# Optimization experiments

Hardware: AMD Instinct MI355X
Metric: run time of the kernel (lower is better)

## Reference

```python
import jax, jax.numpy as jnp
import numpy as np

N = 100000      # nodes
E = 1600000     # edges (avg degree 16)
IN = 512        # input feature dim
H, C = 8, 8     # conv1: 8 heads x 8 channels (hardcoded in module)
HID = H * C     # 64
OUT = 64        # output classes (conv2: 1 head, no concat)
NEG_SLOPE = 0.2 # PyG GATConv default leaky-relu slope


def setup_inputs() -> dict:
    key = jax.random.key(0)
    ks = jax.random.split(key, 10)
    x = jax.random.normal(ks[0], (N, IN), dtype=jnp.float32)
    edge_index = jax.random.randint(ks[1], (2, E), 0, N, dtype=jnp.int32)
    W1 = jax.random.normal(ks[2], (IN, HID), dtype=jnp.float32) / np.sqrt(IN).astype(np.float32)
    a_src1 = jax.random.normal(ks[3], (H, C), dtype=jnp.float32) * 0.1
    a_dst1 = jax.random.normal(ks[4], (H, C), dtype=jnp.float32) * 0.1
    b1 = jnp.zeros((HID,), dtype=jnp.float32)
    W2 = jax.random.normal(ks[5], (HID, OUT), dtype=jnp.float32) / np.sqrt(HID).astype(np.float32)
    a_src2 = jax.random.normal(ks[6], (1, OUT), dtype=jnp.float32) * 0.1
    a_dst2 = jax.random.normal(ks[7], (1, OUT), dtype=jnp.float32) * 0.1
    b2 = jnp.zeros((OUT,), dtype=jnp.float32)
    return {"x": x, "edge_index": edge_index, "W1": W1, "a_src1": a_src1,
            "a_dst1": a_dst1, "b1": b1, "W2": W2, "a_src2": a_src2,
            "a_dst2": a_dst2, "b2": b2}


def _gat_attend(h, src, dst, a_s, a_d, n_nodes):
    """h: [N,H,C]; src/dst: [E]; a_s/a_d: [H,C] -> aggregated [N,H,C]."""
    # per-node half-scores (PyG decomposition of a^T [Wx_i || Wx_j])
    sc_s = jnp.sum(h * a_s, axis=-1)                       # [N,H]
    sc_d = jnp.sum(h * a_d, axis=-1)                       # [N,H]
    logits = jax.nn.leaky_relu(sc_s[src] + sc_d[dst], NEG_SLOPE)  # [E,H]
    # segment softmax over edges grouped by destination node
    mx = jax.ops.segment_max(logits, dst, num_segments=n_nodes)   # [N,H]
    ex = jnp.exp(logits - mx[dst])                          # [E,H]
    denom = jax.ops.segment_sum(ex, dst, num_segments=n_nodes)    # [N,H]
    alpha = ex / (denom[dst] + 1e-16)                       # [E,H]
    msg = h[src] * alpha[:, :, None]                        # [E,H,C]
    return jax.ops.segment_sum(msg, dst, num_segments=n_nodes)    # [N,H,C]


def reference(x, edge_index, W1, a_src1, a_dst1, b1, W2, a_src2, a_dst2, b2):
    n = x.shape[0]
    loop = jnp.arange(n, dtype=edge_index.dtype)
    src = jnp.concatenate([edge_index[0], loop])            # self-loops (PyG default)
    dst = jnp.concatenate([edge_index[1], loop])
    # conv1: 8 heads, concat
    h1 = (x @ W1).reshape(n, H, C)
    o1 = _gat_attend(h1, src, dst, a_src1, a_dst1, n).reshape(n, HID) + b1
    x2 = jax.nn.elu(o1)
    # conv2: 1 head, no concat
    h2 = (x2 @ W2).reshape(n, 1, OUT)
    o2 = _gat_attend(h2, src, dst, a_src2, a_dst2, n)[:, 0] + b2
    return jax.nn.log_softmax(o2, axis=1)
```

## Files before the change

### kernel.cpp

```cpp
#include <hip/hip_runtime.h>
#include <cstdint>
#include <cstddef>

#define LEAKY 0.2f
#define NEG_INF -3.402823466e38f
static const int CHUNK = 2048;

typedef __attribute__((ext_vector_type(8))) short short8;
typedef __attribute__((ext_vector_type(4))) float floatx4;

__device__ __forceinline__ float dot4(float4 a, float4 b) {
    return a.x * b.x + a.y * b.y + a.z * b.z + a.w * b.w;
}

__device__ __forceinline__ unsigned short f2bf(float f) {
    unsigned u = __float_as_uint(f);
    u += 0x7fffu + ((u >> 16) & 1u);
    return (unsigned short)(u >> 16);
}
__device__ __forceinline__ float bf2f(unsigned short u) {
    return __uint_as_float(((unsigned)u) << 16);
}
__device__ __forceinline__ float bflo(unsigned u) { return __uint_as_float(u << 16); }
__device__ __forceinline__ float bfhi(unsigned u) { return __uint_as_float(u & 0xffff0000u); }

__global__ __launch_bounds__(256) void k_init_deg(int* __restrict__ deg, int Nn) {
    int i = blockIdx.x * 256 + threadIdx.x;
    if (i < Nn) deg[i] = 1;
}

__global__ __launch_bounds__(256) void k_count_p(const int* __restrict__ ei, int* __restrict__ deg,
                                                 int E, int Nn) {
    int part = blockIdx.x & 7;
    int lo = (int)((long long)Nn * part >> 3);
    int hi = (int)((long long)Nn * (part + 1) >> 3);
    int nthr = (gridDim.x >> 3) * 256;
    int tid = (blockIdx.x >> 3) * 256 + threadIdx.x;
    for (int e = tid; e < E; e += nthr) {
        int d = ei[E + e];
        if (d >= lo && d < hi) atomicAdd(&deg[d], 1);
    }
}

__global__ __launch_bounds__(256) void k_scan1(const int* __restrict__ deg, int* __restrict__ bsum, int Nn) {
    __shared__ int sm[256];
    int b = blockIdx.x, t = threadIdx.x;
    int s = 0;
    int i0 = b * CHUNK + t * 8;
#pragma unroll
    for (int j = 0; j < 8; ++j) { int i = i0 + j; if (i < Nn) s += deg[i]; }
    sm[t] = s;
    __syncthreads();
    for (int o = 128; o; o >>= 1) { if (t < o) sm[t] += sm[t + o]; __syncthreads(); }
    if (t == 0) bsum[b] = sm[0];
}

__global__ void k_scan2(const int* __restrict__ bsum, int* __restrict__ bpre, int B) {
    int l = threadIdx.x;
    int v = (l < B) ? bsum[l] : 0;
    int inc = v;
#pragma unroll
    for (int o = 1; o < 64; o <<= 1) { int u = __shfl_up(inc, o); if (l >= o) inc += u; }
    if (l < B) bpre[l] = inc - v;
}

__global__ __launch_bounds__(256) void k_scan3(const int* __restrict__ deg, const int* __restrict__ bpre,
                                               int* __restrict__ indptr, int* __restrict__ cursor, int Nn) {
    __shared__ int wsum[4];
    int b = blockIdx.x, t = threadIdx.x, lane = t & 63, w = t >> 6;
    int i0 = b * CHUNK + t * 8;
    int d[8]; int s = 0;
#pragma unroll
    for (int j = 0; j < 8; ++j) { int i = i0 + j; d[j] = (i < Nn) ? deg[i] : 0; s += d[j]; }
    int inc = s;
#pragma unroll
    for (int o = 1; o < 64; o <<= 1) { int u = __shfl_up(inc, o); if (lane >= o) inc += u; }
    if (lane == 63) wsum[w] = inc;
    __syncthreads();
    int wofs = 0;
    for (int k = 0; k < w; ++k) wofs += wsum[k];
    int base = bpre[b] + wofs + (inc - s);
    int run = 0;
#pragma unroll
    for (int j = 0; j < 8; ++j) {
        int i = i0 + j;
        if (i < Nn) {
            int v = base + run;
            indptr[i] = v; cursor[i] = v;
            run += d[j];
            if (i == Nn - 1) indptr[Nn] = v + d[j];
        }
    }
}

__global__ __launch_bounds__(256) void k_fill_p(const int* __restrict__ ei, int* __restrict__ cursor,
                                                int* __restrict__ csr, int E, int Nn) {
    int part = blockIdx.x & 7;
    int lo = (int)((long long)Nn * part >> 3);
    int hi = (int)((long long)Nn * (part + 1) >> 3);
    int nthr = (gridDim.x >> 3) * 256;
    int tid = (blockIdx.x >> 3) * 256 + threadIdx.x;
    int tot = E + Nn;
    for (int idx = tid; idx < tot; idx += nthr) {
        int d = (idx < E) ? ei[E + idx] : idx - E;
        if (d >= lo && d < hi) {
            int s = (idx < E) ? ei[idx] : idx - E;
            int slot = atomicAdd(&cursor[d], 1);
            csr[slot] = s;
        }
    }
}

__global__ __launch_bounds__(256) void k_prepW(const float* __restrict__ W1, unsigned short* __restrict__ W1t) {
    int i = blockIdx.x * 256 + threadIdx.x;
    if (i >= 64 * 512) return;
    int n = i >> 9, k = i & 511;
    W1t[i] = f2bf(W1[k * 64 + n]);
}

__global__ __launch_bounds__(256) void gemm1_mfma(const float* __restrict__ A, const unsigned short* __restrict__ W1t,
                                                  unsigned short* __restrict__ C, int M) {
    __shared__ __align__(16) unsigned short As[128][40];
    __shared__ __align__(16) unsigned short Bs[64][40];
    int t = threadIdx.x;
    int w = t >> 6, l = t & 63;
    int quad = l >> 4, lm = l & 15;
    int row0 = blockIdx.x * 128;

    floatx4 acc[2][4] = {};

    for (int k0 = 0; k0 < 512; k0 += 32) {
#pragma unroll
        for (int j = 0; j < 4; ++j) {
            int f = t + 256 * j;
            int r = f >> 3, c4 = f & 7;
            int rg = row0 + r; if (rg >= M) rg = M - 1;
            float4 v = *(const float4*)(A + (size_t)rg * 512 + k0 + c4 * 4);
            ushort4 b; b.x = f2bf(v.x); b.y = f2bf(v.y); b.z = f2bf(v.z); b.w = f2bf(v.w);
            *(ushort4*)&As[r][c4 * 4] = b;
        }
        {
            int n = t >> 2, seg = t & 3;
            *(uint4*)&Bs[n][seg * 8] = *(const uint4*)(W1t + (size_t)n * 512 + k0 + seg * 8);
        }
        __syncthreads();

        short8 af[2], bfm[4];
#pragma unroll
        for (int tm = 0; tm < 2; ++tm) {
            int m = w * 32 + tm * 16 + lm;
            af[tm] = *(const short8*)&As[m][quad * 8];
        }
#pragma unroll
        for (int tn = 0; tn < 4; ++tn) {
            int n = tn * 16 + lm;
            bfm[tn] = *(const short8*)&Bs[n][quad * 8];
        }
#pragma unroll
        for (int tm = 0; tm < 2; ++tm)
#pragma unroll
            for (int tn = 0; tn < 4; ++tn)
                acc[tm][tn] = __builtin_amdgcn_mfma_f32_16x16x32_bf16(af[tm], bfm[tn], acc[tm][tn], 0, 0, 0);
        __syncthreads();
    }

#pragma unroll
    for (int tm = 0; tm < 2; ++tm) {
#pragma unroll
        for (int r = 0; r < 4; ++r) {
            int row = row0 + w * 32 + tm * 16 + quad * 4 + r;
            if (row < M) {
#pragma unroll
                for (int tn = 0; tn < 4; ++tn)
                    C[(size_t)row * 64 + tn * 16 + lm] = f2bf(acc[tm][tn][r]);
            }
        }
    }
}

template <int KB>
__global__ __launch_bounds__(256) void gemm_n64(const float* __restrict__ A, const float* __restrict__ B,
                                                unsigned short* __restrict__ C, int M, int K) {
    __shared__ float As[KB][68];
    __shared__ float Bs[KB][68];
    int tid = threadIdx.x;
    int row0 = blockIdx.x * 64;
    int tx = tid & 15, ty = tid >> 4;
    float acc[4][4] = {};
    for (int k0 = 0; k0 < K; k0 += KB) {
#pragma unroll
        for (int j = 0; j < (64 * KB) / (256 * 4); ++j) {
            int f = tid + 256 * j;
            int r = f / (KB / 4);
            int c4 = f % (KB / 4);
            int rg = row0 + r; if (rg >= M) rg = M - 1;
            float4 v = *(const float4*)(A + (size_t)rg * K + k0 + c4 * 4);
            As[c4 * 4 + 0][r] = v.x; As[c4 * 4 + 1][r] = v.y;
            As[c4 * 4 + 2][r] = v.z; As[c4 * 4 + 3][r] = v.w;
        }
#pragma unroll
        for (int j = 0; j < (KB * 64) / (256 * 4); ++j) {
            int f = tid + 256 * j;
            int kk = f / 16, c4 = f % 16;
            *(float4*)&Bs[kk][c4 * 4] = *(const float4*)(B + (size_t)(k0 + kk) * 64 + c4 * 4);
        }
        __syncthreads();
#pragma unroll
        for (int kk = 0; kk < KB; ++kk) {
            float4 a = *(const float4*)&As[kk][ty * 4];
            float4 b = *(const float4*)&Bs[kk][tx * 4];
            float av[4] = {a.x, a.y, a.z, a.w};
            float bv[4] = {b.x, b.y, b.z, b.w};
#pragma unroll
            for (int i = 0; i < 4; ++i)
#pragma unroll
                for (int j = 0; j < 4; ++j) acc[i][j] += av[i] * bv[j];
        }
        __syncthreads();
    }
#pragma unroll
    for (int i = 0; i < 4; ++i) {
        int rg = row0 + ty * 4 + i;
        if (rg < M) {
            ushort4 b; b.x = f2bf(acc[i][0]); b.y = f2bf(acc[i][1]);
            b.z = f2bf(acc[i][2]); b.w = f2bf(acc[i][3]);
            *(ushort4*)(C + (size_t)rg * 64 + tx * 4) = b;
        }
    }
}

__global__ __launch_bounds__(256) void k_sc1(const unsigned short* __restrict__ h1, const float* __restrict__ as1,
                                             const float* __restrict__ ad1, float* __restrict__ scs,
                                             float* __restrict__ scd, int Nn) {
    int i = blockIdx.x * 256 + threadIdx.x;
    if (i >= Nn * 8) return;
    int h = i & 7;
    ushort4 p0 = *(const ushort4*)(h1 + (size_t)i * 8);
    ushort4 p1 = *(const ushort4*)(h1 + (size_t)i * 8 + 4);
    float4 v0 = make_float4(bf2f(p0.x), bf2f(p0.y), bf2f(p0.z), bf2f(p0.w));
    float4 v1 = make_float4(bf2f(p1.x), bf2f(p1.y), bf2f(p1.z), bf2f(p1.w));
    const float4* asp = (const float4*)(as1 + h * 8);
    const float4* adp = (const float4*)(ad1 + h * 8);
    scs[i] = dot4(v0, asp[0]) + dot4(v1, asp[1]);
    scd[i] = dot4(v0, adp[0]) + dot4(v1, adp[1]);
}

__global__ __launch_bounds__(256) void k_sc2(const unsigned short* __restrict__ h2, const float* __restrict__ as2,
                                             const float* __restrict__ ad2, float* __restrict__ scs,
                                             float* __restrict__ scd, int Nn) {
    int wave = (blockIdx.x * 256 + threadIdx.x) >> 6;
    int lane = threadIdx.x & 63;
    if (wave >= Nn) return;
    float v = bf2f(h2[(size_t)wave * 64 + lane]);
    float ss = v * as2[lane], sd = v * ad2[lane];
#pragma unroll
    for (int o = 32; o; o >>= 1) { ss += __shfl_xor(ss, o); sd += __shfl_xor(sd, o); }
    if (lane == 0) { scs[wave] = ss; scd[wave] = sd; }
}

__global__ __launch_bounds__(256) void k_agg1(const unsigned short* __restrict__ h1, const float* __restrict__ scs,
                                              const float* __restrict__ scd, const int* __restrict__ indptr,
                                              const int* __restrict__ csr, const float* __restrict__ b1,
                                              float* __restrict__ x2, int Nn) {
    int node = (blockIdx.x * 256 + threadIdx.x) >> 6;
    int l = threadIdx.x & 63;
    if (node >= Nn) return;
    int h8 = l & 7, grp = l >> 3;
    int start = indptr[node], end = indptr[node + 1];
    float sd = scd[node * 8 + h8];

    float mx = NEG_INF;
    float dsum = 0.f;
    float acc8[8] = {};
    for (int base = start; base < end; base += 64) {
        int e = base + l;
        int s64 = csr[e < end ? e : start];
        int cnt = min(64, end - base);
        int nb = (cnt + 7) >> 3;
        float vv[8];
        int sbv[8];
        float lmax = NEG_INF;
#pragma unroll
        for (int b = 0; b < 8; ++b) {
            if (b < nb) {
                int slot = base + b * 8 + grp;
                int sb = __shfl(s64, b * 8 + grp);
                sbv[b] = sb;
                float v = scs[sb * 8 + h8] + sd;
                v = v > 0.f ? v : LEAKY * v;
                vv[b] = (slot < end) ? v : NEG_INF;
                lmax = fmaxf(lmax, vv[b]);
            }
        }
#pragma unroll
        for (int o = 8; o < 64; o <<= 1) lmax = fmaxf(lmax, __shfl_xor(lmax, o));
        float nm = fmaxf(mx, lmax);
        if (base > start && nm > mx) {
            float f = __expf(mx - nm);
            dsum *= f;
#pragma unroll
            for (int k = 0; k < 8; ++k) acc8[k] *= f;
        }
        mx = nm;
#pragma unroll
        for (int b = 0; b < 8; ++b) {
            if (b < nb) {
                float ex = __expf(vv[b] - mx);
                dsum += ex;
                uint4 q = *(const uint4*)(h1 + (size_t)sbv[b] * 64 + h8 * 8);
                acc8[0] += ex * bflo(q.x); acc8[1] += ex * bfhi(q.x);
                acc8[2] += ex * bflo(q.y); acc8[3] += ex * bfhi(q.y);
                acc8[4] += ex * bflo(q.z); acc8[5] += ex * bfhi(q.z);
                acc8[6] += ex * bflo(q.w); acc8[7] += ex * bfhi(q.w);
            }
        }
    }
#pragma unroll
    for (int o = 8; o < 64; o <<= 1) {
        dsum += __shfl_xor(dsum, o);
#pragma unroll
        for (int k = 0; k < 8; ++k) acc8[k] += __shfl_xor(acc8[k], o);
    }
    if (grp == 0) {
        float inv = 1.f / (dsum + 1e-16f);
        float4 ba = *((const float4*)b1 + h8 * 2);
        float4 bb = *((const float4*)b1 + h8 * 2 + 1);
        float o0 = acc8[0] * inv + ba.x, o1 = acc8[1] * inv + ba.y;
        float o2 = acc8[2] * inv + ba.z, o3 = acc8[3] * inv + ba.w;
        float o4 = acc8[4] * inv + bb.x, o5 = acc8[5] * inv + bb.y;
        float o6 = acc8[6] * inv + bb.z, o7 = acc8[7] * inv + bb.w;
        o0 = o0 > 0.f ? o0 : expm1f(o0); o1 = o1 > 0.f ? o1 : expm1f(o1);
        o2 = o2 > 0.f ? o2 : expm1f(o2); o3 = o3 > 0.f ? o3 : expm1f(o3);
        o4 = o4 > 0.f ? o4 : expm1f(o4); o5 = o5 > 0.f ? o5 : expm1f(o5);
        o6 = o6 > 0.f ? o6 : expm1f(o6); o7 = o7 > 0.f ? o7 : expm1f(o7);
        float* dst = x2 + (size_t)node * 64 + h8 * 8;
        *(float4*)dst = make_float4(o0, o1, o2, o3);
        *(float4*)(dst + 4) = make_float4(o4, o5, o6, o7);
    }
}

__global__ __launch_bounds__(256) void k_agg2(const unsigned short* __restrict__ h2, const float* __restrict__ scs,
                                              const float* __restrict__ scd, const int* __restrict__ indptr,
                                              const int* __restrict__ csr, const float* __restrict__ b2,
                                              float* __restrict__ out, int Nn) {
    int node = (blockIdx.x * 256 + threadIdx.x) >> 6;
    int l = threadIdx.x & 63;
    if (node >= Nn) return;
    int g = l >> 3, c8 = l & 7;
    int start = indptr[node], end = indptr[node + 1];
    float sd = scd[node];

    float mx = NEG_INF;
    float dsum = 0.f;
    float acc8[8] = {};
    for (int base = start; base < end; base += 64) {
        int e = base + l;
        int s64 = csr[e < end ? e : start];
        float v = scs[s64] + sd;
        v = v > 0.f ? v : LEAKY * v;
        v = (e < end) ? v : NEG_INF;
        float lmax = v;
#pragma unroll
        for (int o = 32; o; o >>= 1) lmax = fmaxf(lmax, __shfl_xor(lmax, o));
        float nm = fmaxf(mx, lmax);
        if (base > start && nm > mx) {
            float f = __expf(mx - nm);
            dsum *= f;
#pragma unroll
            for (int k = 0; k < 8; ++k) acc8[k] *= f;
        }
        mx = nm;
        float ex = (e < end) ? __expf(v - mx) : 0.f;
        dsum += ex;
        int cnt = min(64, end - base);
        int nb = (cnt + 7) >> 3;
#pragma unroll 2
        for (int b = 0; b < nb; ++b) {
            float exv = __shfl(ex, b * 8 + g);
            int sb = __shfl(s64, b * 8 + g);
            uint4 q = *(const uint4*)(h2 + (size_t)sb * 64 + c8 * 8);
            acc8[0] += exv * bflo(q.x); acc8[1] += exv * bfhi(q.x);
            acc8[2] += exv * bflo(q.y); acc8[3] += exv * bfhi(q.y);
            acc8[4] += exv * bflo(q.z); acc8[5] += exv * bfhi(q.z);
            acc8[6] += exv * bflo(q.w); acc8[7] += exv * bfhi(q.w);
        }
    }
#pragma unroll
    for (int o = 32; o; o >>= 1) dsum += __shfl_xor(dsum, o);
#pragma unroll
    for (int o = 8; o < 64; o <<= 1)
#pragma unroll
        for (int k = 0; k < 8; ++k) acc8[k] += __shfl_xor(acc8[k], o);

    float inv = 1.f / (dsum + 1e-16f);
    float4 ba = *((const float4*)b2 + c8 * 2);
    float4 bb = *((const float4*)b2 + c8 * 2 + 1);
    float ov[8];
    ov[0] = acc8[0] * inv + ba.x; ov[1] = acc8[1] * inv + ba.y;
    ov[2] = acc8[2] * inv + ba.z; ov[3] = acc8[3] * inv + ba.w;
    ov[4] = acc8[4] * inv + bb.x; ov[5] = acc8[5] * inv + bb.y;
    ov[6] = acc8[6] * inv + bb.z; ov[7] = acc8[7] * inv + bb.w;

    float m2 = ov[0];
#pragma unroll
    for (int k = 1; k < 8; ++k) m2 = fmaxf(m2, ov[k]);
#pragma unroll
    for (int o = 1; o < 8; o <<= 1) m2 = fmaxf(m2, __shfl_xor(m2, o));
    float se = 0.f;
#pragma unroll
    for (int k = 0; k < 8; ++k) se += __expf(ov[k] - m2);
#pragma unroll
    for (int o = 1; o < 8; o <<= 1) se += __shfl_xor(se, o);
    float ls = m2 + __logf(se);
    if (g == 0) {
        float* dst = out + (size_t)node * 64 + c8 * 8;
        *(float4*)dst = make_float4(ov[0] - ls, ov[1] - ls, ov[2] - ls, ov[3] - ls);
        *(float4*)(dst + 4) = make_float4(ov[4] - ls, ov[5] - ls, ov[6] - ls, ov[7] - ls);
    }
}

extern "C" void kernel_launch(void* const* d_in, const int* in_sizes, int n_in,
                              void* d_out, int out_size, void* d_ws, size_t ws_size,
                              hipStream_t stream) {
    (void)n_in; (void)out_size; (void)ws_size;
    const float* x   = (const float*)d_in[0];
    const int*   ei  = (const int*)d_in[1];
    const float* W1  = (const float*)d_in[2];
    const float* as1 = (const float*)d_in[3];
    const float* ad1 = (const float*)d_in[4];
    const float* b1  = (const float*)d_in[5];
    const float* W2  = (const float*)d_in[6];
    const float* as2 = (const float*)d_in[7];
    const float* ad2 = (const float*)d_in[8];
    const float* b2  = (const float*)d_in[9];
    float* out = (float*)d_out;

    const int N = in_sizes[0] / 512;
    const int E = in_sizes[1] / 2;

    char* p = (char*)d_ws;
    auto alloc = [&](size_t bytes) -> char* {
        char* r = p; p += (bytes + 255) & ~(size_t)255; return r;
    };
    unsigned short* h1bf = (unsigned short*)alloc((size_t)N * 64 * 2);
    float* x2    = (float*)alloc((size_t)N * 64 * 4);
    unsigned short* h2bf = h1bf;
    float* sc1s  = (float*)alloc((size_t)N * 8 * 4);
    float* sc1d  = (float*)alloc((size_t)N * 8 * 4);
    float* sc2s  = (float*)alloc((size_t)N * 4);
    float* sc2d  = (float*)alloc((size_t)N * 4);
    int*   deg   = (int*)alloc((size_t)N * 4);
    int*   cursor= (int*)alloc((size_t)N * 4);
    int*   indptr= (int*)alloc((size_t)(N + 1) * 4);
    int*   csr   = (int*)alloc((size_t)(E + N) * 4);
    int*   bsum  = (int*)alloc(64 * 4);
    int*   bpre  = (int*)alloc(64 * 4);
    unsigned short* W1t = (unsigned short*)alloc(64 * 512 * 2);

    const int B = (N + CHUNK - 1) / CHUNK;

    k_init_deg<<<(N + 255) / 256, 256, 0, stream>>>(deg, N);
    k_count_p<<<1024, 256, 0, stream>>>(ei, deg, E, N);
    k_scan1  <<<B, 256, 0, stream>>>(deg, bsum, N);
    k_scan2  <<<1, 64, 0, stream>>>(bsum, bpre, B);
    k_scan3  <<<B, 256, 0, stream>>>(deg, bpre, indptr, cursor, N);
    k_fill_p <<<1024, 256, 0, stream>>>(ei, cursor, csr, E, N);

    k_prepW<<<(64 * 512 + 255) / 256, 256, 0, stream>>>(W1, W1t);
    gemm1_mfma<<<(N + 127) / 128, 256, 0, stream>>>(x, W1t, h1bf, N);
    k_sc1 <<<(N * 8 + 255) / 256, 256, 0, stream>>>(h1bf, as1, ad1, sc1s, sc1d, N);
    k_agg1<<<(N + 3) / 4, 256, 0, stream>>>(h1bf, sc1s, sc1d, indptr, csr, b1, x2, N);

    gemm_n64<64><<<(N + 63) / 64, 256, 0, stream>>>(x2, W2, h2bf, N, 64);
    k_sc2 <<<(N + 3) / 4, 256, 0, stream>>>(h2bf, as2, ad2, sc2s, sc2d, N);
    k_agg2<<<(N + 3) / 4, 256, 0, stream>>>(h2bf, sc2s, sc2d, indptr, csr, b2, out, N);
}
```

Baseline: 640.5 us.

## Fuse conv2 GEMM and score computation into layer-1 aggregation; drop LDS staging

Fuses the second linear layer (x2 @ W2) and the conv2 attention half-scores into the layer-1 aggregation kernel. Each wave now computes its node's 64-wide h2 row from the post-ELU features via shuffles against W2 held in LDS, which removes the fp32 x2 round-trip and two kernel launches. The block-prefix scan is folded into k_scan3, dropping k_scan2. gemm1 now loads A and B fragments straight from global memory into MFMA operands with no LDS staging or barriers, at the cost of less coalesced loads and each block reloading W2 into LDS.

```diff
diff --git a/kernel.cpp b/kernel.cpp
--- a/kernel.cpp
+++ b/kernel.cpp
@@ -23,6 +23,15 @@
 }
 __device__ __forceinline__ float bflo(unsigned u) { return __uint_as_float(u << 16); }
 __device__ __forceinline__ float bfhi(unsigned u) { return __uint_as_float(u & 0xffff0000u); }
+
+__device__ __forceinline__ short8 pack8(float4 a, float4 b) {
+    short8 r;
+    r[0] = (short)f2bf(a.x); r[1] = (short)f2bf(a.y);
+    r[2] = (short)f2bf(a.z); r[3] = (short)f2bf(a.w);
+    r[4] = (short)f2bf(b.x); r[5] = (short)f2bf(b.y);
+    r[6] = (short)f2bf(b.z); r[7] = (short)f2bf(b.w);
+    return r;
+}
 
 __global__ __launch_bounds__(256) void k_init_deg(int* __restrict__ deg, int Nn) {
     int i = blockIdx.x * 256 + threadIdx.x;
@@ -55,19 +64,18 @@
     if (t == 0) bsum[b] = sm[0];
 }
 
-__global__ void k_scan2(const int* __restrict__ bsum, int* __restrict__ bpre, int B) {
-    int l = threadIdx.x;
-    int v = (l < B) ? bsum[l] : 0;
-    int inc = v;
-#pragma unroll
-    for (int o = 1; o < 64; o <<= 1) { int u = __shfl_up(inc, o); if (l >= o) inc += u; }
-    if (l < B) bpre[l] = inc - v;
-}
-
-__global__ __launch_bounds__(256) void k_scan3(const int* __restrict__ deg, const int* __restrict__ bpre,
-                                               int* __restrict__ indptr, int* __restrict__ cursor, int Nn) {
+__global__ __launch_bounds__(256) void k_scan3(const int* __restrict__ deg, const int* __restrict__ bsum,
+                                               int* __restrict__ indptr, int* __restrict__ cursor,
+                                               int Nn, int B) {
     __shared__ int wsum[4];
     int b = blockIdx.x, t = threadIdx.x, lane = t & 63, w = t >> 6;
+
+    int vb = (lane < B) ? bsum[lane] : 0;
+    int incb = vb;
+#pragma unroll
+    for (int o = 1; o < 64; o <<= 1) { int u = __shfl_up(incb, o); if (lane >= o) incb += u; }
+    int bpre_b = __shfl(incb - vb, b);
+
     int i0 = b * CHUNK + t * 8;
     int d[8]; int s = 0;
 #pragma unroll
@@ -79,7 +87,7 @@
     __syncthreads();
     int wofs = 0;
     for (int k = 0; k < w; ++k) wofs += wsum[k];
-    int base = bpre[b] + wofs + (inc - s);
+    int base = bpre_b + wofs + (inc - s);
     int run = 0;
 #pragma unroll
     for (int j = 0; j < 8; ++j) {
@@ -120,111 +128,48 @@
 
 __global__ __launch_bounds__(256) void gemm1_mfma(const float* __restrict__ A, const unsigned short* __restrict__ W1t,
                                                   unsigned short* __restrict__ C, int M) {
-    __shared__ __align__(16) unsigned short As[128][40];
-    __shared__ __align__(16) unsigned short Bs[64][40];
     int t = threadIdx.x;
     int w = t >> 6, l = t & 63;
     int quad = l >> 4, lm = l & 15;
-    int row0 = blockIdx.x * 128;
+    int rowbase = blockIdx.x * 128 + w * 32;
+
+    int r0 = rowbase + lm;       if (r0 >= M) r0 = M - 1;
+    int r1 = rowbase + 16 + lm;  if (r1 >= M) r1 = M - 1;
+    const float* a0 = A + (size_t)r0 * 512 + quad * 8;
+    const float* a1 = A + (size_t)r1 * 512 + quad * 8;
+    const unsigned short* bp = W1t + (size_t)lm * 512 + quad * 8;
 
     floatx4 acc[2][4] = {};
 
+#pragma unroll 2
     for (int k0 = 0; k0 < 512; k0 += 32) {
-#pragma unroll
-        for (int j = 0; j < 4; ++j) {
-            int f = t + 256 * j;
-            int r = f >> 3, c4 = f & 7;
-            int rg = row0 + r; if (rg >= M) rg = M - 1;
-            float4 v = *(const float4*)(A + (size_t)rg * 512 + k0 + c4 * 4);
-            ushort4 b; b.x = f2bf(v.x); b.y = f2bf(v.y); b.z = f2bf(v.z); b.w = f2bf(v.w);
-            *(ushort4*)&As[r][c4 * 4] = b;
-        }
-        {
-            int n = t >> 2, seg = t & 3;
-            *(uint4*)&Bs[n][seg * 8] = *(const uint4*)(W1t + (size_t)n * 512 + k0 + seg * 8);
-        }
-        __syncthreads();
-
-        short8 af[2], bfm[4];
-#pragma unroll
-        for (int tm = 0; tm < 2; ++tm) {
-            int m = w * 32 + tm * 16 + lm;
-            af[tm] = *(const short8*)&As[m][quad * 8];
-        }
+        float4 va0 = *(const float4*)(a0 + k0);
+        float4 vb0 = *(const float4*)(a0 + k0 + 4);
+        float4 va1 = *(const float4*)(a1 + k0);
+        float4 vb1 = *(const float4*)(a1 + k0 + 4);
+        short8 bfm[4];
+#pragma unroll
+        for (int tn = 0; tn < 4; ++tn)
+            bfm[tn] = *(const short8*)(bp + (size_t)tn * 16 * 512 + k0);
+        short8 af0 = pack8(va0, vb0);
+        short8 af1 = pack8(va1, vb1);
 #pragma unroll
         for (int tn = 0; tn < 4; ++tn) {
-            int n = tn * 16 + lm;
-            bfm[tn] = *(const short8*)&Bs[n][quad * 8];
-        }
-#pragma unroll
-        for (int tm = 0; tm < 2; ++tm)
-#pragma unroll
-            for (int tn = 0; tn < 4; ++tn)
-                acc[tm][tn] = __builtin_amdgcn_mfma_f32_16x16x32_bf16(af[tm], bfm[tn], acc[tm][tn], 0, 0, 0);
-        __syncthreads();
+            acc[0][tn] = __builtin_amdgcn_mfma_f32_16x16x32_bf16(af0, bfm[tn], acc[0][tn], 0, 0, 0);
+            acc[1][tn] = __builtin_amdgcn_mfma_f32_16x16x32_bf16(af1, bfm[tn], acc[1][tn], 0, 0, 0);
+        }
     }
 
 #pragma unroll
     for (int tm = 0; tm < 2; ++tm) {
 #pragma unroll
         for (int r = 0; r < 4; ++r) {
-            int row = row0 + w * 32 + tm * 16 + quad * 4 + r;
+            int row = rowbase + tm * 16 + quad * 4 + r;
             if (row < M) {
 #pragma unroll
                 for (int tn = 0; tn < 4; ++tn)
                     C[(size_t)row * 64 + tn * 16 + lm] = f2bf(acc[tm][tn][r]);
             }
-        }
-    }
-}
-
-template <int KB>
-__global__ __launch_bounds__(256) void gemm_n64(const float* __restrict__ A, const float* __restrict__ B,
-                                                unsigned short* __restrict__ C, int M, int K) {
-    __shared__ float As[KB][68];
-    __shared__ float Bs[KB][68];
-    int tid = threadIdx.x;
-    int row0 = blockIdx.x * 64;
-    int tx = tid & 15, ty = tid >> 4;
-    float acc[4][4] = {};
-    for (int k0 = 0; k0 < K; k0 += KB) {
-#pragma unroll
-        for (int j = 0; j < (64 * KB) / (256 * 4); ++j) {
-            int f = tid + 256 * j;
-            int r = f / (KB / 4);
-            int c4 = f % (KB / 4);
-            int rg = row0 + r; if (rg >= M) rg = M - 1;
-            float4 v = *(const float4*)(A + (size_t)rg * K + k0 + c4 * 4);
-            As[c4 * 4 + 0][r] = v.x; As[c4 * 4 + 1][r] = v.y;
-            As[c4 * 4 + 2][r] = v.z; As[c4 * 4 + 3][r] = v.w;
-        }
-#pragma unroll
-        for (int j = 0; j < (KB * 64) / (256 * 4); ++j) {
-            int f = tid + 256 * j;
-            int kk = f / 16, c4 = f % 16;
-            *(float4*)&Bs[kk][c4 * 4] = *(const float4*)(B + (size_t)(k0 + kk) * 64 + c4 * 4);
-        }
-        __syncthreads();
-#pragma unroll
-        for (int kk = 0; kk < KB; ++kk) {
-            float4 a = *(const float4*)&As[kk][ty * 4];
-            float4 b = *(const float4*)&Bs[kk][tx * 4];
-            float av[4] = {a.x, a.y, a.z, a.w};
-            float bv[4] = {b.x, b.y, b.z, b.w};
-#pragma unroll
-            for (int i = 0; i < 4; ++i)
-#pragma unroll
-                for (int j = 0; j < 4; ++j) acc[i][j] += av[i] * bv[j];
-        }
-        __syncthreads();
-    }
-#pragma unroll
-    for (int i = 0; i < 4; ++i) {
-        int rg = row0 + ty * 4 + i;
-        if (rg < M) {
-            ushort4 b; b.x = f2bf(acc[i][0]); b.y = f2bf(acc[i][1]);
-            b.z = f2bf(acc[i][2]); b.w = f2bf(acc[i][3]);
-            *(ushort4*)(C + (size_t)rg * 64 + tx * 4) = b;
         }
     }
 }
@@ -245,25 +190,23 @@
     scd[i] = dot4(v0, adp[0]) + dot4(v1, adp[1]);
 }
 
-__global__ __launch_bounds__(256) void k_sc2(const unsigned short* __restrict__ h2, const float* __restrict__ as2,
-                                             const float* __restrict__ ad2, float* __restrict__ scs,
-                                             float* __restrict__ scd, int Nn) {
-    int wave = (blockIdx.x * 256 + threadIdx.x) >> 6;
-    int lane = threadIdx.x & 63;
-    if (wave >= Nn) return;
-    float v = bf2f(h2[(size_t)wave * 64 + lane]);
-    float ss = v * as2[lane], sd = v * ad2[lane];
-#pragma unroll
-    for (int o = 32; o; o >>= 1) { ss += __shfl_xor(ss, o); sd += __shfl_xor(sd, o); }
-    if (lane == 0) { scs[wave] = ss; scd[wave] = sd; }
-}
-
-__global__ __launch_bounds__(256) void k_agg1(const unsigned short* __restrict__ h1, const float* __restrict__ scs,
-                                              const float* __restrict__ scd, const int* __restrict__ indptr,
-                                              const int* __restrict__ csr, const float* __restrict__ b1,
-                                              float* __restrict__ x2, int Nn) {
-    int node = (blockIdx.x * 256 + threadIdx.x) >> 6;
-    int l = threadIdx.x & 63;
+__global__ __launch_bounds__(256) void k_agg1f(const unsigned short* __restrict__ h1, const float* __restrict__ scs,
+                                               const float* __restrict__ scd, const int* __restrict__ indptr,
+                                               const int* __restrict__ csr, const float* __restrict__ b1,
+                                               const float* __restrict__ W2, const float* __restrict__ as2,
+                                               const float* __restrict__ ad2, unsigned short* __restrict__ h2,
+                                               float* __restrict__ sc2s, float* __restrict__ sc2d, int Nn) {
+    __shared__ float W2s[64][64];
+    int t = threadIdx.x;
+#pragma unroll
+    for (int j = 0; j < 4; ++j) {
+        int f = t + 256 * j;
+        *(float4*)&W2s[f >> 4][(f & 15) * 4] = *(const float4*)(W2 + (size_t)f * 4);
+    }
+    __syncthreads();
+
+    int node = (blockIdx.x * 256 + t) >> 6;
+    int l = t & 63;
     if (node >= Nn) return;
     int h8 = l & 7, grp = l >> 3;
     int start = indptr[node], end = indptr[node + 1];
@@ -321,22 +264,32 @@
 #pragma unroll
         for (int k = 0; k < 8; ++k) acc8[k] += __shfl_xor(acc8[k], o);
     }
-    if (grp == 0) {
-        float inv = 1.f / (dsum + 1e-16f);
-        float4 ba = *((const float4*)b1 + h8 * 2);
-        float4 bb = *((const float4*)b1 + h8 * 2 + 1);
-        float o0 = acc8[0] * inv + ba.x, o1 = acc8[1] * inv + ba.y;
-        float o2 = acc8[2] * inv + ba.z, o3 = acc8[3] * inv + ba.w;
-        float o4 = acc8[4] * inv + bb.x, o5 = acc8[5] * inv + bb.y;
-        float o6 = acc8[6] * inv + bb.z, o7 = acc8[7] * inv + bb.w;
-        o0 = o0 > 0.f ? o0 : expm1f(o0); o1 = o1 > 0.f ? o1 : expm1f(o1);
-        o2 = o2 > 0.f ? o2 : expm1f(o2); o3 = o3 > 0.f ? o3 : expm1f(o3);
-        o4 = o4 > 0.f ? o4 : expm1f(o4); o5 = o5 > 0.f ? o5 : expm1f(o5);
-        o6 = o6 > 0.f ? o6 : expm1f(o6); o7 = o7 > 0.f ? o7 : expm1f(o7);
-        float* dst = x2 + (size_t)node * 64 + h8 * 8;
-        *(float4*)dst = make_float4(o0, o1, o2, o3);
-        *(float4*)(dst + 4) = make_float4(o4, o5, o6, o7);
-    }
+    float inv = 1.f / (dsum + 1e-16f);
+    float4 ba = *((const float4*)b1 + h8 * 2);
+    float4 bb = *((const float4*)b1 + h8 * 2 + 1);
+    float o8[8];
+    o8[0] = acc8[0] * inv + ba.x; o8[1] = acc8[1] * inv + ba.y;
+    o8[2] = acc8[2] * inv + ba.z; o8[3] = acc8[3] * inv + ba.w;
+    o8[4] = acc8[4] * inv + bb.x; o8[5] = acc8[5] * inv + bb.y;
+    o8[6] = acc8[6] * inv + bb.z; o8[7] = acc8[7] * inv + bb.w;
+#pragma unroll
+    for (int k = 0; k < 8; ++k) o8[k] = o8[k] > 0.f ? o8[k] : expm1f(o8[k]);
+
+    float hacc = 0.f;
+#pragma unroll
+    for (int j = 0; j < 8; ++j) {
+#pragma unroll
+        for (int g = 0; g < 8; ++g) {
+            float xv = __shfl(o8[j], g);
+            hacc = fmaf(xv, W2s[g * 8 + j][l], hacc);
+        }
+    }
+    h2[(size_t)node * 64 + l] = f2bf(hacc);
+
+    float ss = hacc * as2[l], sdd = hacc * ad2[l];
+#pragma unroll
+    for (int o = 32; o; o >>= 1) { ss += __shfl_xor(ss, o); sdd += __shfl_xor(sdd, o); }
+    if (l == 0) { sc2s[node] = ss; sc2d[node] = sdd; }
 }
 
 __global__ __launch_bounds__(256) void k_agg2(const unsigned short* __restrict__ h2, const float* __restrict__ scs,
@@ -443,8 +396,7 @@
         char* r = p; p += (bytes + 255) & ~(size_t)255; return r;
     };
     unsigned short* h1bf = (unsigned short*)alloc((size_t)N * 64 * 2);
-    float* x2    = (float*)alloc((size_t)N * 64 * 4);
-    unsigned short* h2bf = h1bf;
+    unsigned short* h2bf = (unsigned short*)alloc((size_t)N * 64 * 2);
     float* sc1s  = (float*)alloc((size_t)N * 8 * 4);
     float* sc1d  = (float*)alloc((size_t)N * 8 * 4);
     float* sc2s  = (float*)alloc((size_t)N * 4);
@@ -454,7 +406,6 @@
     int*   indptr= (int*)alloc((size_t)(N + 1) * 4);
     int*   csr   = (int*)alloc((size_t)(E + N) * 4);
     int*   bsum  = (int*)alloc(64 * 4);
-    int*   bpre  = (int*)alloc(64 * 4);
     unsigned short* W1t = (unsigned short*)alloc(64 * 512 * 2);
 
     const int B = (N + CHUNK - 1) / CHUNK;
@@ -462,16 +413,15 @@
     k_init_deg<<<(N + 255) / 256, 256, 0, stream>>>(deg, N);
     k_count_p<<<1024, 256, 0, stream>>>(ei, deg, E, N);
     k_scan1  <<<B, 256, 0, stream>>>(deg, bsum, N);
-    k_scan2  <<<1, 64, 0, stream>>>(bsum, bpre, B);
-    k_scan3  <<<B, 256, 0, stream>>>(deg, bpre, indptr, cursor, N);
+    k_scan3  <<<B, 256, 0, stream>>>(deg, bsum, indptr, cursor, N, B);
     k_fill_p <<<1024, 256, 0, stream>>>(ei, cursor, csr, E, N);
 
     k_prepW<<<(64 * 512 + 255) / 256, 256, 0, stream>>>(W1, W1t);
     gemm1_mfma<<<(N + 127) / 128, 256, 0, stream>>>(x, W1t, h1bf, N);
     k_sc1 <<<(N * 8 + 255) / 256, 256, 0, stream>>>(h1bf, as1, ad1, sc1s, sc1d, N);
-    k_agg1<<<(N + 3) / 4, 256, 0, stream>>>(h1bf, sc1s, sc1d, indptr, csr, b1, x2, N);
-
-    gemm_n64<64><<<(N + 63) / 64, 256, 0, stream>>>(x2, W2, h2bf, N, 64);
-    k_sc2 <<<(N + 3) / 4, 256, 0, stream>>>(h2bf, as2, ad2, sc2s, sc2d, N);
+
+    k_agg1f<<<(N + 3) / 4, 256, 0, stream>>>(h1bf, sc1s, sc1d, indptr, csr, b1,
+                                             W2, as2, ad2, h2bf, sc2s, sc2d, N);
+
     k_agg2<<<(N + 3) / 4, 256, 0, stream>>>(h2bf, sc2s, sc2d, indptr, csr, b2, out, N);
 }
```

New measurement: 703.5 us. 9.8% more time.
